# Optimization experiments

Measured on AMD Instinct MI355X. Metric: run time of the kernel, lower is better.

## Reference

```python
import jax, jax.numpy as jnp
import numpy as np

HEADS = 8
DIM_HEAD = 64

def setup_inputs() -> dict:
    key = jax.random.key(0)
    ks = jax.random.split(key, 5)
    B, N, D = 2, 4096, 512  # query_dim = inner_dim = 512
    s = 0.02
    return {
        "x": jax.random.normal(ks[0], (B, N, D), dtype=jnp.float32),
        "Wq": jax.random.normal(ks[1], (D, D), dtype=jnp.float32) * s,
        "Wk": jax.random.normal(ks[2], (D, D), dtype=jnp.float32) * s,
        "Wv": jax.random.normal(ks[3], (D, D), dtype=jnp.float32) * s,
        "Wo": jax.random.normal(ks[4], (D, D), dtype=jnp.float32) * s,
        "bo": jnp.zeros((D,), dtype=jnp.float32),
    }

def reference(x, Wq, Wk, Wv, Wo, bo):
    B, N, D = x.shape
    h, dh = HEADS, DIM_HEAD
    scale = dh ** (-0.5)
    # self-attention: context = x
    q = x @ Wq  # [B, N, h*dh]
    k = x @ Wk
    v = x @ Wv
    # b n (h d) -> b h n d
    q = q.reshape(B, N, h, dh).transpose(0, 2, 1, 3)
    k = k.reshape(B, N, h, dh).transpose(0, 2, 1, 3)
    v = v.reshape(B, N, h, dh).transpose(0, 2, 1, 3)
    sim = jnp.einsum('bhid,bhjd->bhij', q, k) * scale  # full [B,h,N,N] matrix
    attn = jax.nn.softmax(sim, axis=-1)
    out = jnp.einsum('bhij,bhjd->bhid', attn, v)
    out = out.transpose(0, 2, 1, 3).reshape(B, N, h * dh)
    return out @ Wo + bo
```

## Files before the change

### kernel.cpp

```cpp
#include <hip/hip_runtime.h>
#include <hip/hip_bf16.h>
#include <stddef.h>
#include <stdint.h>

typedef __bf16 bf16_t;
typedef bf16_t bf16x8 __attribute__((ext_vector_type(8)));
typedef bf16_t bf16x4 __attribute__((ext_vector_type(4)));
typedef bf16_t bf16x2 __attribute__((ext_vector_type(2)));
typedef float floatx4 __attribute__((ext_vector_type(4)));
typedef float floatx16 __attribute__((ext_vector_type(16)));
typedef int   intx4  __attribute__((ext_vector_type(4)));

#define SEQ    4096
#define DMODEL 512
#define NH     8
#define BATCH  2
#define QSCALE 0.18033688011112042f

__device__ __forceinline__ void ld_lds16(const void* g, void* l) {
  __builtin_amdgcn_global_load_lds(
      (const __attribute__((address_space(1))) unsigned int*)g,
      (__attribute__((address_space(3))) unsigned int*)l, 16, 0, 0);
}

__global__ __launch_bounds__(256) void prep_k(
    const float* __restrict__ x,
    const float* __restrict__ W0, const float* __restrict__ W1,
    const float* __restrict__ W2, const float* __restrict__ W3,
    bf16_t* __restrict__ Wt, bf16_t* __restrict__ xb)
{
  if (blockIdx.z == 4) {
    const floatx4* xf = (const floatx4*)x;
    bf16x4* xo = (bf16x4*)xb;
    int base = (blockIdx.y * 16 + blockIdx.x) * 4096 + threadIdx.x;
    #pragma unroll
    for (int i = 0; i < 16; i++) {
      floatx4 v = xf[base + i * 256];
      xo[base + i * 256] = bf16x4{(bf16_t)v.x, (bf16_t)v.y, (bf16_t)v.z, (bf16_t)v.w};
    }
    return;
  }
  __shared__ float Ws[32][33];
  const float* W = (blockIdx.z == 0) ? W0 : (blockIdx.z == 1) ? W1
                 : (blockIdx.z == 2) ? W2 : W3;
  bf16_t* out = Wt + (size_t)blockIdx.z * DMODEL * DMODEL;
  const int tx = threadIdx.x & 31, ty = threadIdx.x >> 5;
  const int k0 = blockIdx.y * 32, n0 = blockIdx.x * 32;
  #pragma unroll
  for (int i = 0; i < 4; i++) {
    int kk = ty + i * 8;
    Ws[kk][tx] = W[(size_t)(k0 + kk) * DMODEL + n0 + tx];
  }
  __syncthreads();
  #pragma unroll
  for (int i = 0; i < 4; i++) {
    int nn = ty + i * 8;
    out[(size_t)(n0 + nn) * DMODEL + k0 + tx] = (bf16_t)Ws[tx][nn];
  }
}

__global__ __launch_bounds__(256) void qkv_k(
    const bf16_t* __restrict__ xb, const bf16_t* __restrict__ Wt,
    bf16_t* __restrict__ Qw, bf16_t* __restrict__ Ksw, bf16_t* __restrict__ Vsw)
{
  __shared__ __align__(16) char smem[2 * 2048 * 16];
  const int tid  = threadIdx.x;
  const int wave = tid >> 6;
  const int lane = tid & 63;
  const int lh   = lane >> 4, lm = lane & 15;
  const int bm   = blockIdx.x * 128;
  const int mode = blockIdx.y >> 2;
  const int hp   = blockIdx.y & 3;
  const bf16_t* Wm = Wt + (size_t)mode * DMODEL * DMODEL;
  const int bn   = hp * 128;

  int offA[4], ldsA[4], offB[4], ldsB[4];
  #pragma unroll
  for (int i = 0; i < 4; i++) {
    int S = i * 256 + wave * 64 + lane;
    int r = S >> 3, cc = (S & 7) ^ (r & 7);
    offA[i] = (bm + r) * DMODEL + cc * 8;
    ldsA[i] = (i * 256 + wave * 64) * 16;
    int n = S >> 3, cb = (S & 7) ^ (n & 7);
    offB[i] = (bn + n) * DMODEL + cb * 8;
    ldsB[i] = (1024 + i * 256 + wave * 64) * 16;
  }

  floatx4 acc[2][8];
  #pragma unroll
  for (int rb = 0; rb < 2; rb++)
    #pragma unroll
    for (int nb = 0; nb < 8; nb++) acc[rb][nb] = floatx4{0.f, 0.f, 0.f, 0.f};

  auto issue = [&](int kt, int buf) {
    char* bp = smem + buf * 2048 * 16;
    #pragma unroll
    for (int i = 0; i < 4; i++) {
      ld_lds16(xb + offA[i] + kt * 64, bp + ldsA[i]);
      ld_lds16(Wm + offB[i] + kt * 64, bp + ldsB[i]);
    }
  };

  issue(0, 0);
  for (int kt = 0; kt < 8; kt++) {
    __syncthreads();
    if (kt < 7) issue(kt + 1, (kt + 1) & 1);
    const char* bp = smem + (kt & 1) * 2048 * 16;
    #pragma unroll
    for (int ks = 0; ks < 2; ks++) {
      int cc = ks * 4 + lh;
      int rA = wave * 32 + lm;
      bf16x8 a0 = *(const bf16x8*)(bp + (rA * 8 + (cc ^ (rA & 7))) * 16);
      bf16x8 a1 = *(const bf16x8*)(bp + ((rA + 16) * 8 + (cc ^ (rA & 7))) * 16);
      #pragma unroll
      for (int nb = 0; nb < 8; nb++) {
        int n = nb * 16 + lm;
        bf16x8 b = *(const bf16x8*)(bp + (1024 + n * 8 + (cc ^ (n & 7))) * 16);
        acc[0][nb] = __builtin_amdgcn_mfma_f32_16x16x32_bf16(a0, b, acc[0][nb], 0, 0, 0);
        acc[1][nb] = __builtin_amdgcn_mfma_f32_16x16x32_bf16(a1, b, acc[1][nb], 0, 0, 0);
      }
    }
  }

  if (mode == 0) {
    #pragma unroll
    for (int rb = 0; rb < 2; rb++)
      #pragma unroll
      for (int nb = 0; nb < 8; nb++)
        #pragma unroll
        for (int r = 0; r < 4; r++) {
          int row = bm + wave * 32 + rb * 16 + lh * 4 + r;
          Qw[(size_t)row * DMODEL + bn + nb * 16 + lm] =
              (bf16_t)(acc[rb][nb][r] * QSCALE);
        }
  } else if (mode == 1) {
    #pragma unroll
    for (int rb = 0; rb < 2; rb++)
      #pragma unroll
      for (int nb = 0; nb < 8; nb++) {
        int col = bn + nb * 16 + lm;
        int h = col >> 6, d = col & 63;
        #pragma unroll
        for (int r = 0; r < 4; r++) {
          int row = bm + wave * 32 + rb * 16 + lh * 4 + r;
          int bb = row >> 12, tk = row & 4095;
          size_t off = ((size_t)(bb * NH + h) * 64 + (tk >> 6)) * 4096
                     + (size_t)(tk & 63) * 64
                     + ((((d >> 3) ^ (tk & 7)) << 3) | (d & 7));
          Ksw[off] = (bf16_t)acc[rb][nb][r];
        }
      }
  } else {
    __syncthreads();
    bf16_t (*Ts)[136] = (bf16_t(*)[136])smem;
    #pragma unroll
    for (int rb = 0; rb < 2; rb++)
      #pragma unroll
      for (int nb = 0; nb < 8; nb++) {
        int dloc = nb * 16 + lm, tok0 = wave * 32 + rb * 16 + lh * 4;
        bf16x4 v = {(bf16_t)acc[rb][nb][0], (bf16_t)acc[rb][nb][1],
                    (bf16_t)acc[rb][nb][2], (bf16_t)acc[rb][nb][3]};
        *(bf16x4*)&Ts[dloc][tok0] = v;
      }
    __syncthreads();
    const int bb = bm >> 12, tk0 = bm & 4095;
    #pragma unroll
    for (int i = 0; i < 8; i++) {
      int idx = tid + i * 256;
      int dl = idx >> 4, c8 = idx & 15;
      int col = bn + dl, h = col >> 6, d = col & 63;
      bf16x8 val = *(bf16x8*)&Ts[dl][c8 * 8];
      int cw = c8 & 7;
      int g = cw >> 1, sub = cw & 1;
      size_t tbase = (((size_t)(bb * NH + h) * 64) + (tk0 >> 6) + (c8 >> 3)) * 4096
                   + (size_t)d * 64;
      bf16x4 v0 = {val[0], val[1], val[2], val[3]};
      bf16x4 v1 = {val[4], val[5], val[6], val[7]};
      *(bf16x4*)&Vsw[tbase + (((2 * g) ^ (d & 7)) << 3) + sub * 4] = v0;
      *(bf16x4*)&Vsw[tbase + (((2 * g + 1) ^ (d & 7)) << 3) + sub * 4] = v1;
    }
  }
}

__global__ __launch_bounds__(256) void out_k(
    const bf16_t* __restrict__ A, const bf16_t* __restrict__ Wt,
    const float* __restrict__ bias, float* __restrict__ out)
{
  __shared__ __align__(16) char smem[2 * 1536 * 16];
  const int tid  = threadIdx.x;
  const int wave = tid >> 6;
  const int lane = tid & 63;
  const int lh   = lane >> 4, lm = lane & 15;
  const int bm   = blockIdx.x * 128;
  const int bn   = blockIdx.y * 64;

  int offA[4], ldsA[4];
  #pragma unroll
  for (int i = 0; i < 4; i++) {
    int S = i * 256 + wave * 64 + lane;
    int r = S >> 3, cc = (S & 7) ^ (r & 7);
    offA[i] = (bm + r) * DMODEL + cc * 8;
    ldsA[i] = (i * 256 + wave * 64) * 16;
  }
  int offB[2], ldsB[2];
  #pragma unroll
  for (int j = 0; j < 2; j++) {
    int S = j * 256 + wave * 64 + lane;
    int n = S >> 3, cc = (S & 7) ^ (n & 7);
    offB[j] = (bn + n) * DMODEL + cc * 8;
    ldsB[j] = (1024 + j * 256 + wave * 64) * 16;
  }

  floatx4 acc[2][4];
  #pragma unroll
  for (int rb = 0; rb < 2; rb++)
    #pragma unroll
    for (int nb = 0; nb < 4; nb++) acc[rb][nb] = floatx4{0.f, 0.f, 0.f, 0.f};

  auto issue = [&](int kt, int buf) {
    char* bp = smem + buf * 1536 * 16;
    #pragma unroll
    for (int i = 0; i < 4; i++) ld_lds16(A + offA[i] + kt * 64, bp + ldsA[i]);
    #pragma unroll
    for (int j = 0; j < 2; j++) ld_lds16(Wt + offB[j] + kt * 64, bp + ldsB[j]);
  };

  issue(0, 0);
  for (int kt = 0; kt < 8; kt++) {
    __syncthreads();
    if (kt < 7) issue(kt + 1, (kt + 1) & 1);
    const char* bp = smem + (kt & 1) * 1536 * 16;
    #pragma unroll
    for (int ks = 0; ks < 2; ks++) {
      int cc = ks * 4 + lh;
      int rA = wave * 32 + lm;
      bf16x8 a0 = *(const bf16x8*)(bp + (rA * 8 + (cc ^ (rA & 7))) * 16);
      bf16x8 a1 = *(const bf16x8*)(bp + ((rA + 16) * 8 + (cc ^ (rA & 7))) * 16);
      #pragma unroll
      for (int nb = 0; nb < 4; nb++) {
        int n = nb * 16 + lm;
        bf16x8 b = *(const bf16x8*)(bp + (1024 + n * 8 + (cc ^ (n & 7))) * 16);
        acc[0][nb] = __builtin_amdgcn_mfma_f32_16x16x32_bf16(a0, b, acc[0][nb], 0, 0, 0);
        acc[1][nb] = __builtin_amdgcn_mfma_f32_16x16x32_bf16(a1, b, acc[1][nb], 0, 0, 0);
      }
    }
  }

  #pragma unroll
  for (int rb = 0; rb < 2; rb++)
    #pragma unroll
    for (int nb = 0; nb < 4; nb++) {
      float bv = bias[bn + nb * 16 + lm];
      #pragma unroll
      for (int r = 0; r < 4; r++) {
        int row = bm + wave * 32 + rb * 16 + lh * 4 + r;
        out[(size_t)row * DMODEL + bn + nb * 16 + lm] = acc[rb][nb][r] + bv;
      }
    }
}

__global__ __launch_bounds__(512, 4) void attn_k(
    const bf16_t* __restrict__ Qw, const bf16_t* __restrict__ Ksw,
    const bf16_t* __restrict__ Vsw, bf16_t* __restrict__ Ow)
{
  __shared__ __align__(16) char smem[2 * 32768];
  const int tid  = threadIdx.x;
  const int wave = tid >> 6;
  const int qh   = wave >> 1;
  const int kh   = wave & 1;
  const int lane = tid & 63;
  const int hi   = lane >> 5;
  const int lo   = lane & 31;
  const int bh   = blockIdx.y, b = bh >> 3, h = bh & 7;
  const int q0   = blockIdx.x * 128;
  const size_t kvbase = (size_t)bh * 64 * 4096;

  const int qrow_g = b * SEQ + q0 + qh * 32 + lo;
  bf16x8 qreg[4];
  #pragma unroll
  for (int i = 0; i < 4; i++)
    qreg[i] = *(const bf16x8*)&Qw[(size_t)qrow_g * DMODEL + h * 64 + i * 16 + hi * 8];

  floatx16 accO[2];
  #pragma unroll
  for (int nbo = 0; nbo < 2; nbo++)
    #pragma unroll
    for (int j = 0; j < 16; j++) accO[nbo][j] = 0.f;
  float ls = 0.f;

  auto issue = [&](int s, int buf) {
    char* bp = smem + buf * 32768;
    const bf16_t* k0 = Ksw + kvbase + (size_t)(2 * s) * 4096;
    const bf16_t* v0 = Vsw + kvbase + (size_t)(2 * s) * 4096;
    const bf16_t* k1 = k0 + 4096;
    const bf16_t* v1 = v0 + 4096;
    ld_lds16(k0 + tid * 8, bp + tid * 16);
    ld_lds16(v0 + tid * 8, bp + 8192 + tid * 16);
    ld_lds16(k1 + tid * 8, bp + 16384 + tid * 16);
    ld_lds16(v1 + tid * 8, bp + 24576 + tid * 16);
  };

  issue(0, 0);
  for (int s = 0; s < SEQ / 128; s++) {
    __syncthreads();
    if (s < SEQ / 128 - 1) issue(s + 1, (s + 1) & 1);
    const bf16_t* Kb = (const bf16_t*)(smem + (s & 1) * 32768 + kh * 16384);
    const bf16_t* Vb = Kb + 4096;

    floatx16 accS[2];
    #pragma unroll
    for (int nb = 0; nb < 2; nb++)
      #pragma unroll
      for (int j = 0; j < 16; j++) accS[nb][j] = 0.f;
    #pragma unroll
    for (int kd = 0; kd < 4; kd++) {
      #pragma unroll
      for (int nb = 0; nb < 2; nb++) {
        int row = nb * 32 + lo;
        bf16x8 ak = *(const bf16x8*)&Kb[row * 64 + (((kd * 2 + hi) ^ (row & 7)) << 3)];
        accS[nb] = __builtin_amdgcn_mfma_f32_32x32x16_bf16(ak, qreg[kd], accS[nb], 0, 0, 0);
      }
    }

    int pk[2][8];
    #pragma unroll
    for (int nb = 0; nb < 2; nb++) {
      float p[16];
      #pragma unroll
      for (int r = 0; r < 16; r++) p[r] = __builtin_amdgcn_exp2f(accS[nb][r]);
      #pragma unroll
      for (int r = 0; r < 16; r += 4)
        ls += (p[r] + p[r + 1]) + (p[r + 2] + p[r + 3]);
      #pragma unroll
      for (int i = 0; i < 8; i++) {
        bf16x2 t2 = {(bf16_t)p[2 * i], (bf16_t)p[2 * i + 1]};
        pk[nb][i] = __builtin_bit_cast(int, t2);
      }
    }

    #pragma unroll
    for (int c = 0; c < 4; c++) {
      intx4 pi = {pk[c >> 1][4 * (c & 1)],     pk[c >> 1][4 * (c & 1) + 1],
                  pk[c >> 1][4 * (c & 1) + 2], pk[c >> 1][4 * (c & 1) + 3]};
      bf16x8 pf = __builtin_bit_cast(bf16x8, pi);
      #pragma unroll
      for (int nbo = 0; nbo < 2; nbo++) {
        int row = nbo * 32 + lo;
        bf16x8 av = *(const bf16x8*)&Vb[row * 64 + (((c * 2 + hi) ^ (row & 7)) << 3)];
        accO[nbo] = __builtin_amdgcn_mfma_f32_32x32x16_bf16(av, pf, accO[nbo], 0, 0, 0);
      }
    }
  }

  ls += __shfl_xor(ls, 32, 64);
  __syncthreads();
  float* mrg = (float*)smem;
  if (kh == 1) {
    #pragma unroll
    for (int nbo = 0; nbo < 2; nbo++) {
      float* dst = mrg + qh * 2048 + nbo * 1024 + lane * 16;
      #pragma unroll
      for (int g = 0; g < 4; g++) {
        floatx4 v = {accO[nbo][4 * g], accO[nbo][4 * g + 1],
                     accO[nbo][4 * g + 2], accO[nbo][4 * g + 3]};
        *(floatx4*)(dst + 4 * g) = v;
      }
    }
    if (hi == 0) mrg[8192 + qh * 32 + lo] = ls;
  }
  __syncthreads();
  if (kh == 0) {
    float linv = 1.0f / (ls + mrg[8192 + qh * 32 + lo]);
    #pragma unroll
    for (int nbo = 0; nbo < 2; nbo++) {
      const float* src = mrg + qh * 2048 + nbo * 1024 + lane * 16;
      #pragma unroll
      for (int g = 0; g < 4; g++) {
        floatx4 v = *(const floatx4*)(src + 4 * g);
        accO[nbo][4 * g]     += v.x;
        accO[nbo][4 * g + 1] += v.y;
        accO[nbo][4 * g + 2] += v.z;
        accO[nbo][4 * g + 3] += v.w;
      }
    }
    bf16_t* Os = (bf16_t*)(smem + 36864 + qh * 4096);
    #pragma unroll
    for (int nbo = 0; nbo < 2; nbo++)
      #pragma unroll
      for (int g = 0; g < 4; g++) {
        int dbase = g * 8 + 4 * hi + 32 * nbo;
        bf16x4 v4 = {(bf16_t)(accO[nbo][4 * g] * linv),
                     (bf16_t)(accO[nbo][4 * g + 1] * linv),
                     (bf16_t)(accO[nbo][4 * g + 2] * linv),
                     (bf16_t)(accO[nbo][4 * g + 3] * linv)};
        *(bf16x4*)&Os[lo * 64 + (dbase ^ ((lo & 7) << 3))] = v4;
      }
    #pragma unroll
    for (int i = 0; i < 4; i++) {
      int idx = i * 64 + lane;
      int q = idx >> 3, c8 = idx & 7;
      bf16x8 v = *(const bf16x8*)&Os[q * 64 + ((c8 ^ (q & 7)) << 3)];
      int row_g = b * SEQ + q0 + qh * 32 + q;
      *(bf16x8*)&Ow[(size_t)row_g * DMODEL + h * 64 + c8 * 8] = v;
    }
  }
}

extern "C" void kernel_launch(void* const* d_in, const int* in_sizes, int n_in,
                              void* d_out, int out_size, void* d_ws, size_t ws_size,
                              hipStream_t stream)
{
  const float* x  = (const float*)d_in[0];
  const float* Wq = (const float*)d_in[1];
  const float* Wk = (const float*)d_in[2];
  const float* Wv = (const float*)d_in[3];
  const float* Wo = (const float*)d_in[4];
  const float* bo = (const float*)d_in[5];
  float* out = (float*)d_out;

  const int M = BATCH * SEQ;
  const size_t WT = (size_t)DMODEL * DMODEL;
  const size_t E  = (size_t)M * DMODEL;
  if (ws_size < (4 * WT + 3 * E) * sizeof(bf16_t)) return;

  bf16_t* Wt  = (bf16_t*)d_ws;
  bf16_t* Qw  = Wt + 4 * WT;
  bf16_t* Ksw = Qw + E;
  bf16_t* Vsw = Ksw + E;
  bf16_t* Ow  = Qw;
  bf16_t* xbf = (bf16_t*)d_out;

  prep_k<<<dim3(16, 16, 5), 256, 0, stream>>>(x, Wq, Wk, Wv, Wo, Wt, xbf);

  qkv_k<<<dim3(M / 128, 12), 256, 0, stream>>>(xbf, Wt, Qw, Ksw, Vsw);

  attn_k<<<dim3(SEQ / 128, BATCH * NH), 512, 0, stream>>>(Qw, Ksw, Vsw, Ow);

  out_k<<<dim3(M / 128, DMODEL / 64), 256, 0, stream>>>(Ow, Wt + 3 * WT, bo, out);
}
```

Measured before the change: 174.6 us.

## Shrink GEMM K-tile to 32, swap operands for transposed K/V epilogues

Both projection GEMMs now stage 32-wide K slices (16 iterations) instead of 64, halving LDS per buffer, which can raise occupancy. In the QKV kernel, Q and K blocks swap the A/B operands so each lane's accumulators hold contiguous feature columns, allowing vector bf16x4 stores into the swizzled layouts. The V path drops its LDS transpose stage and writes directly with a permuted token position. The attention merge buffer is padded to stride 20 to avoid bank conflicts, at the cost of scalar LDS accesses and more barrier iterations.

```diff
diff --git a/kernel.cpp b/kernel.cpp
--- a/kernel.cpp
+++ b/kernel.cpp
@@ -63,27 +63,28 @@
     const bf16_t* __restrict__ xb, const bf16_t* __restrict__ Wt,
     bf16_t* __restrict__ Qw, bf16_t* __restrict__ Ksw, bf16_t* __restrict__ Vsw)
 {
-  __shared__ __align__(16) char smem[2 * 2048 * 16];
+  __shared__ __align__(16) char smem[2 * 16384];
   const int tid  = threadIdx.x;
   const int wave = tid >> 6;
   const int lane = tid & 63;
   const int lh   = lane >> 4, lm = lane & 15;
-  const int bm   = blockIdx.x * 128;
+  const int bx   = blockIdx.x;
   const int mode = blockIdx.y >> 2;
   const int hp   = blockIdx.y & 3;
   const bf16_t* Wm = Wt + (size_t)mode * DMODEL * DMODEL;
-  const int bn   = hp * 128;
-
-  int offA[4], ldsA[4], offB[4], ldsB[4];
-  #pragma unroll
-  for (int i = 0; i < 4; i++) {
-    int S = i * 256 + wave * 64 + lane;
-    int r = S >> 3, cc = (S & 7) ^ (r & 7);
-    offA[i] = (bm + r) * DMODEL + cc * 8;
-    ldsA[i] = (i * 256 + wave * 64) * 16;
-    int n = S >> 3, cb = (S & 7) ^ (n & 7);
-    offB[i] = (bn + n) * DMODEL + cb * 8;
-    ldsB[i] = (1024 + i * 256 + wave * 64) * 16;
+  const bool SW  = (mode != 2);
+  const bf16_t* srcA = SW ? (Wm + (size_t)hp * 128 * DMODEL)
+                          : (xb + (size_t)bx * 128 * DMODEL);
+  const bf16_t* srcB = SW ? (xb + (size_t)bx * 128 * DMODEL)
+                          : (Wm + (size_t)hp * 128 * DMODEL);
+
+  int offR[2], ldsO[2];
+  #pragma unroll
+  for (int i = 0; i < 2; i++) {
+    int S = i * 256 + tid;
+    int r = S >> 2, bc = S & 3, cc = bc ^ (r & 3);
+    offR[i] = r * DMODEL + cc * 8;
+    ldsO[i] = (i * 256 + wave * 64) * 16;
   }
 
   floatx4 acc[2][8];
@@ -93,92 +94,75 @@
     for (int nb = 0; nb < 8; nb++) acc[rb][nb] = floatx4{0.f, 0.f, 0.f, 0.f};
 
   auto issue = [&](int kt, int buf) {
-    char* bp = smem + buf * 2048 * 16;
-    #pragma unroll
-    for (int i = 0; i < 4; i++) {
-      ld_lds16(xb + offA[i] + kt * 64, bp + ldsA[i]);
-      ld_lds16(Wm + offB[i] + kt * 64, bp + ldsB[i]);
+    char* bp = smem + buf * 16384;
+    #pragma unroll
+    for (int i = 0; i < 2; i++) {
+      ld_lds16(srcA + offR[i] + kt * 32, bp + ldsO[i]);
+      ld_lds16(srcB + offR[i] + kt * 32, bp + 8192 + ldsO[i]);
     }
   };
 
   issue(0, 0);
-  for (int kt = 0; kt < 8; kt++) {
+  for (int kt = 0; kt < 16; kt++) {
     __syncthreads();
-    if (kt < 7) issue(kt + 1, (kt + 1) & 1);
-    const char* bp = smem + (kt & 1) * 2048 * 16;
-    #pragma unroll
-    for (int ks = 0; ks < 2; ks++) {
-      int cc = ks * 4 + lh;
-      int rA = wave * 32 + lm;
-      bf16x8 a0 = *(const bf16x8*)(bp + (rA * 8 + (cc ^ (rA & 7))) * 16);
-      bf16x8 a1 = *(const bf16x8*)(bp + ((rA + 16) * 8 + (cc ^ (rA & 7))) * 16);
+    if (kt < 15) issue(kt + 1, (kt + 1) & 1);
+    const char* bp = smem + (kt & 1) * 16384;
+    int rA = wave * 32 + lm;
+    bf16x8 a0 = *(const bf16x8*)(bp + (rA * 4 + (lh ^ (rA & 3))) * 16);
+    bf16x8 a1 = *(const bf16x8*)(bp + ((rA + 16) * 4 + (lh ^ (rA & 3))) * 16);
+    #pragma unroll
+    for (int nb = 0; nb < 8; nb++) {
+      int n = nb * 16 + lm;
+      bf16x8 b = *(const bf16x8*)(bp + 8192 + (n * 4 + (lh ^ (n & 3))) * 16);
+      acc[0][nb] = __builtin_amdgcn_mfma_f32_16x16x32_bf16(a0, b, acc[0][nb], 0, 0, 0);
+      acc[1][nb] = __builtin_amdgcn_mfma_f32_16x16x32_bf16(a1, b, acc[1][nb], 0, 0, 0);
+    }
+  }
+
+  if (mode == 0) {
+    #pragma unroll
+    for (int rb = 0; rb < 2; rb++)
       #pragma unroll
       for (int nb = 0; nb < 8; nb++) {
-        int n = nb * 16 + lm;
-        bf16x8 b = *(const bf16x8*)(bp + (1024 + n * 8 + (cc ^ (n & 7))) * 16);
-        acc[0][nb] = __builtin_amdgcn_mfma_f32_16x16x32_bf16(a0, b, acc[0][nb], 0, 0, 0);
-        acc[1][nb] = __builtin_amdgcn_mfma_f32_16x16x32_bf16(a1, b, acc[1][nb], 0, 0, 0);
-      }
-    }
-  }
-
-  if (mode == 0) {
+        int col0 = hp * 128 + wave * 32 + rb * 16 + lh * 4;
+        int qrow = bx * 128 + nb * 16 + lm;
+        bf16x4 v = {(bf16_t)(acc[rb][nb][0] * QSCALE), (bf16_t)(acc[rb][nb][1] * QSCALE),
+                    (bf16_t)(acc[rb][nb][2] * QSCALE), (bf16_t)(acc[rb][nb][3] * QSCALE)};
+        *(bf16x4*)&Qw[(size_t)qrow * DMODEL + col0] = v;
+      }
+  } else if (mode == 1) {
     #pragma unroll
     for (int rb = 0; rb < 2; rb++)
       #pragma unroll
-      for (int nb = 0; nb < 8; nb++)
-        #pragma unroll
-        for (int r = 0; r < 4; r++) {
-          int row = bm + wave * 32 + rb * 16 + lh * 4 + r;
-          Qw[(size_t)row * DMODEL + bn + nb * 16 + lm] =
-              (bf16_t)(acc[rb][nb][r] * QSCALE);
-        }
-  } else if (mode == 1) {
-    #pragma unroll
-    for (int rb = 0; rb < 2; rb++)
-      #pragma unroll
       for (int nb = 0; nb < 8; nb++) {
-        int col = bn + nb * 16 + lm;
-        int h = col >> 6, d = col & 63;
-        #pragma unroll
-        for (int r = 0; r < 4; r++) {
-          int row = bm + wave * 32 + rb * 16 + lh * 4 + r;
-          int bb = row >> 12, tk = row & 4095;
-          size_t off = ((size_t)(bb * NH + h) * 64 + (tk >> 6)) * 4096
-                     + (size_t)(tk & 63) * 64
-                     + ((((d >> 3) ^ (tk & 7)) << 3) | (d & 7));
-          Ksw[off] = (bf16_t)acc[rb][nb][r];
-        }
-      }
-  } else {
-    __syncthreads();
-    bf16_t (*Ts)[136] = (bf16_t(*)[136])smem;
-    #pragma unroll
-    for (int rb = 0; rb < 2; rb++)
-      #pragma unroll
-      for (int nb = 0; nb < 8; nb++) {
-        int dloc = nb * 16 + lm, tok0 = wave * 32 + rb * 16 + lh * 4;
+        int d0g = hp * 128 + wave * 32 + rb * 16 + lh * 4;
+        int h = d0g >> 6, dl = d0g & 63;
+        int key = bx * 128 + nb * 16 + lm;
+        int bb = key >> 12, tk = key & 4095;
+        size_t off = ((size_t)(bb * NH + h) * 64 + (tk >> 6)) * 4096
+                   + (size_t)(tk & 63) * 64
+                   + (((dl >> 3) ^ (tk & 7)) << 3) + (dl & 7);
         bf16x4 v = {(bf16_t)acc[rb][nb][0], (bf16_t)acc[rb][nb][1],
                     (bf16_t)acc[rb][nb][2], (bf16_t)acc[rb][nb][3]};
-        *(bf16x4*)&Ts[dloc][tok0] = v;
-      }
-    __syncthreads();
-    const int bb = bm >> 12, tk0 = bm & 4095;
-    #pragma unroll
-    for (int i = 0; i < 8; i++) {
-      int idx = tid + i * 256;
-      int dl = idx >> 4, c8 = idx & 15;
-      int col = bn + dl, h = col >> 6, d = col & 63;
-      bf16x8 val = *(bf16x8*)&Ts[dl][c8 * 8];
-      int cw = c8 & 7;
-      int g = cw >> 1, sub = cw & 1;
-      size_t tbase = (((size_t)(bb * NH + h) * 64) + (tk0 >> 6) + (c8 >> 3)) * 4096
-                   + (size_t)d * 64;
-      bf16x4 v0 = {val[0], val[1], val[2], val[3]};
-      bf16x4 v1 = {val[4], val[5], val[6], val[7]};
-      *(bf16x4*)&Vsw[tbase + (((2 * g) ^ (d & 7)) << 3) + sub * 4] = v0;
-      *(bf16x4*)&Vsw[tbase + (((2 * g + 1) ^ (d & 7)) << 3) + sub * 4] = v1;
-    }
+        *(bf16x4*)&Ksw[off] = v;
+      }
+  } else {
+    #pragma unroll
+    for (int rb = 0; rb < 2; rb++)
+      #pragma unroll
+      for (int nb = 0; nb < 8; nb++) {
+        int t0 = bx * 128 + wave * 32 + rb * 16 + lh * 4;
+        int bb = t0 >> 12, tt = t0 & 4095, tin = tt & 63;
+        int pos = (tin & ~15) | (((tin >> 2) & 1) << 3) | (((tin >> 3) & 1) << 2);
+        int colg = hp * 128 + nb * 16 + lm;
+        int h = colg >> 6, d = colg & 63;
+        size_t off = ((size_t)(bb * NH + h) * 64 + (tt >> 6)) * 4096
+                   + (size_t)d * 64
+                   + (((pos >> 3) ^ (d & 7)) << 3) + (pos & 7);
+        bf16x4 v = {(bf16_t)acc[rb][nb][0], (bf16_t)acc[rb][nb][1],
+                    (bf16_t)acc[rb][nb][2], (bf16_t)acc[rb][nb][3]};
+        *(bf16x4*)&Vsw[off] = v;
+      }
   }
 }
 
@@ -186,7 +170,7 @@
     const bf16_t* __restrict__ A, const bf16_t* __restrict__ Wt,
     const float* __restrict__ bias, float* __restrict__ out)
 {
-  __shared__ __align__(16) char smem[2 * 1536 * 16];
+  __shared__ __align__(16) char smem[2 * 12288];
   const int tid  = threadIdx.x;
   const int wave = tid >> 6;
   const int lane = tid & 63;
@@ -194,21 +178,20 @@
   const int bm   = blockIdx.x * 128;
   const int bn   = blockIdx.y * 64;
 
-  int offA[4], ldsA[4];
-  #pragma unroll
-  for (int i = 0; i < 4; i++) {
-    int S = i * 256 + wave * 64 + lane;
-    int r = S >> 3, cc = (S & 7) ^ (r & 7);
-    offA[i] = (bm + r) * DMODEL + cc * 8;
-    ldsA[i] = (i * 256 + wave * 64) * 16;
-  }
-  int offB[2], ldsB[2];
-  #pragma unroll
-  for (int j = 0; j < 2; j++) {
-    int S = j * 256 + wave * 64 + lane;
-    int n = S >> 3, cc = (S & 7) ^ (n & 7);
-    offB[j] = (bn + n) * DMODEL + cc * 8;
-    ldsB[j] = (1024 + j * 256 + wave * 64) * 16;
+  int offRA[2], ldsOA[2];
+  #pragma unroll
+  for (int i = 0; i < 2; i++) {
+    int S = i * 256 + tid;
+    int r = S >> 2, bc = S & 3, cc = bc ^ (r & 3);
+    offRA[i] = (bm + r) * DMODEL + cc * 8;
+    ldsOA[i] = (i * 256 + wave * 64) * 16;
+  }
+  int offB, ldsOB;
+  {
+    int S = tid;
+    int n = S >> 2, bc = S & 3, cc = bc ^ (n & 3);
+    offB  = (bn + n) * DMODEL + cc * 8;
+    ldsOB = (512 + wave * 64) * 16;
   }
 
   floatx4 acc[2][4];
@@ -218,31 +201,26 @@
     for (int nb = 0; nb < 4; nb++) acc[rb][nb] = floatx4{0.f, 0.f, 0.f, 0.f};
 
   auto issue = [&](int kt, int buf) {
-    char* bp = smem + buf * 1536 * 16;
-    #pragma unroll
-    for (int i = 0; i < 4; i++) ld_lds16(A + offA[i] + kt * 64, bp + ldsA[i]);
-    #pragma unroll
-    for (int j = 0; j < 2; j++) ld_lds16(Wt + offB[j] + kt * 64, bp + ldsB[j]);
+    char* bp = smem + buf * 12288;
+    #pragma unroll
+    for (int i = 0; i < 2; i++) ld_lds16(A + offRA[i] + kt * 32, bp + ldsOA[i]);
+    ld_lds16(Wt + offB + kt * 32, bp + ldsOB);
   };
 
   issue(0, 0);
-  for (int kt = 0; kt < 8; kt++) {
+  for (int kt = 0; kt < 16; kt++) {
     __syncthreads();
-    if (kt < 7) issue(kt + 1, (kt + 1) & 1);
-    const char* bp = smem + (kt & 1) * 1536 * 16;
-    #pragma unroll
-    for (int ks = 0; ks < 2; ks++) {
-      int cc = ks * 4 + lh;
-      int rA = wave * 32 + lm;
-      bf16x8 a0 = *(const bf16x8*)(bp + (rA * 8 + (cc ^ (rA & 7))) * 16);
-      bf16x8 a1 = *(const bf16x8*)(bp + ((rA + 16) * 8 + (cc ^ (rA & 7))) * 16);
-      #pragma unroll
-      for (int nb = 0; nb < 4; nb++) {
-        int n = nb * 16 + lm;
-        bf16x8 b = *(const bf16x8*)(bp + (1024 + n * 8 + (cc ^ (n & 7))) * 16);
-        acc[0][nb] = __builtin_amdgcn_mfma_f32_16x16x32_bf16(a0, b, acc[0][nb], 0, 0, 0);
-        acc[1][nb] = __builtin_amdgcn_mfma_f32_16x16x32_bf16(a1, b, acc[1][nb], 0, 0, 0);
-      }
+    if (kt < 15) issue(kt + 1, (kt + 1) & 1);
+    const char* bp = smem + (kt & 1) * 12288;
+    int rA = wave * 32 + lm;
+    bf16x8 a0 = *(const bf16x8*)(bp + (rA * 4 + (lh ^ (rA & 3))) * 16);
+    bf16x8 a1 = *(const bf16x8*)(bp + ((rA + 16) * 4 + (lh ^ (rA & 3))) * 16);
+    #pragma unroll
+    for (int nb = 0; nb < 4; nb++) {
+      int n = nb * 16 + lm;
+      bf16x8 b = *(const bf16x8*)(bp + (512 + n * 4 + (lh ^ (n & 3))) * 16);
+      acc[0][nb] = __builtin_amdgcn_mfma_f32_16x16x32_bf16(a0, b, acc[0][nb], 0, 0, 0);
+      acc[1][nb] = __builtin_amdgcn_mfma_f32_16x16x32_bf16(a1, b, acc[1][nb], 0, 0, 0);
     }
   }
 
@@ -292,12 +270,10 @@
     char* bp = smem + buf * 32768;
     const bf16_t* k0 = Ksw + kvbase + (size_t)(2 * s) * 4096;
     const bf16_t* v0 = Vsw + kvbase + (size_t)(2 * s) * 4096;
-    const bf16_t* k1 = k0 + 4096;
-    const bf16_t* v1 = v0 + 4096;
-    ld_lds16(k0 + tid * 8, bp + tid * 16);
-    ld_lds16(v0 + tid * 8, bp + 8192 + tid * 16);
-    ld_lds16(k1 + tid * 8, bp + 16384 + tid * 16);
-    ld_lds16(v1 + tid * 8, bp + 24576 + tid * 16);
+    ld_lds16(k0 + tid * 8,        bp + tid * 16);
+    ld_lds16(v0 + tid * 8,        bp + 8192 + tid * 16);
+    ld_lds16(k0 + 4096 + tid * 8, bp + 16384 + tid * 16);
+    ld_lds16(v0 + 4096 + tid * 8, bp + 24576 + tid * 16);
   };
 
   issue(0, 0);
@@ -358,32 +334,32 @@
   if (kh == 1) {
     #pragma unroll
     for (int nbo = 0; nbo < 2; nbo++) {
-      float* dst = mrg + qh * 2048 + nbo * 1024 + lane * 16;
+      float* dst = mrg + qh * 2720 + nbo * 1360 + lane * 20;
       #pragma unroll
       for (int g = 0; g < 4; g++) {
-        floatx4 v = {accO[nbo][4 * g], accO[nbo][4 * g + 1],
-                     accO[nbo][4 * g + 2], accO[nbo][4 * g + 3]};
-        *(floatx4*)(dst + 4 * g) = v;
-      }
-    }
-    if (hi == 0) mrg[8192 + qh * 32 + lo] = ls;
+        dst[4 * g + 0] = accO[nbo][4 * g + 0];
+        dst[4 * g + 1] = accO[nbo][4 * g + 1];
+        dst[4 * g + 2] = accO[nbo][4 * g + 2];
+        dst[4 * g + 3] = accO[nbo][4 * g + 3];
+      }
+    }
+    if (hi == 0) mrg[10816 + qh * 32 + lo] = ls;
   }
   __syncthreads();
   if (kh == 0) {
-    float linv = 1.0f / (ls + mrg[8192 + qh * 32 + lo]);
+    float linv = 1.0f / (ls + mrg[10816 + qh * 32 + lo]);
     #pragma unroll
     for (int nbo = 0; nbo < 2; nbo++) {
-      const float* src = mrg + qh * 2048 + nbo * 1024 + lane * 16;
+      const float* src = mrg + qh * 2720 + nbo * 1360 + lane * 20;
       #pragma unroll
       for (int g = 0; g < 4; g++) {
-        floatx4 v = *(const floatx4*)(src + 4 * g);
-        accO[nbo][4 * g]     += v.x;
-        accO[nbo][4 * g + 1] += v.y;
-        accO[nbo][4 * g + 2] += v.z;
-        accO[nbo][4 * g + 3] += v.w;
-      }
-    }
-    bf16_t* Os = (bf16_t*)(smem + 36864 + qh * 4096);
+        accO[nbo][4 * g + 0] += src[4 * g + 0];
+        accO[nbo][4 * g + 1] += src[4 * g + 1];
+        accO[nbo][4 * g + 2] += src[4 * g + 2];
+        accO[nbo][4 * g + 3] += src[4 * g + 3];
+      }
+    }
+    bf16_t* Os = (bf16_t*)(smem + 49152 + qh * 4096);
     #pragma unroll
     for (int nbo = 0; nbo < 2; nbo++)
       #pragma unroll
```

Result: slower. 182.8 us (+4.7%).
